# Performance work log

Hardware: AMD Instinct MI355X
Metric: run time of the kernel (lower is better)

## Reference

```python
import jax, jax.numpy as jnp
import numpy as np

B, T, H, C_CLS = 1024, 256, 256, 10
SIGMA = 1.0 / H


def setup_inputs() -> dict:
    key = jax.random.key(0)
    ks = jax.random.split(key, 10)
    n = lambda k, shp: SIGMA * jax.random.normal(k, shp, dtype=jnp.float32)
    return {
        "x": jax.random.normal(ks[0], (B, T), dtype=jnp.float32),
        "W_gx": n(ks[1], (1, H)), "W_gh": n(ks[2], (H, H)), "b_g": jnp.zeros(H, jnp.float32),
        "W_ix": n(ks[3], (1, H)), "W_ih": n(ks[4], (H, H)), "b_i": jnp.zeros(H, jnp.float32),
        "W_fx": n(ks[5], (1, H)), "W_fh": n(ks[6], (H, H)), "b_f": jnp.zeros(H, jnp.float32),
        "W_ox": n(ks[7], (1, H)), "W_oh": n(ks[8], (H, H)), "b_o": jnp.zeros(H, jnp.float32),
        "W_ph": n(ks[9], (H, C_CLS)), "b_p": jnp.zeros(C_CLS, jnp.float32),
    }


def reference(x, W_gx, W_gh, b_g, W_ix, W_ih, b_i, W_fx, W_fh, b_f, W_ox, W_oh, b_o, W_ph, b_p):
    batch = x.shape[0]
    hdim = W_gh.shape[0]

    def step(carry, x_t):
        h, c = carry
        xi = x_t[:, None]  # [B,1] scalar input per step
        g = jnp.tanh(xi @ W_gx + h @ W_gh + b_g)
        i = jax.nn.sigmoid(xi @ W_ix + h @ W_ih + b_i)
        # NOTE: original torch code swaps b_o/b_f in f_t/o_t; preserved faithfully.
        f = jax.nn.sigmoid(xi @ W_fx + h @ W_fh + b_o)
        o = jax.nn.sigmoid(xi @ W_ox + h @ W_oh + b_f)
        c = g * i + c * f
        h = jnp.tanh(c) * o
        return (h, c), None

    h0 = jnp.zeros((batch, hdim), x.dtype)
    c0 = jnp.zeros((batch, hdim), x.dtype)
    (h_T, _), _ = jax.lax.scan(step, (h0, c0), x.T)  # scan over time [T,B]
    # original computes p_t every step but only returns the last one
    return h_T @ W_ph + b_p
```

## Files before the change

kernel.cpp:

```cpp
#include <hip/hip_runtime.h>


#define Bsz   1024
#define Tt    256
#define Hh    256
#define NCLS  10
#define NTHR  512
#define WSPN  32768

typedef float f32x4 __attribute__((ext_vector_type(4)));
typedef short s16x8 __attribute__((ext_vector_type(8)));
typedef unsigned int u32;

__device__ __forceinline__ unsigned short f2bf(float f) {
    u32 u = __builtin_bit_cast(u32, f);
    return (unsigned short)((u + 0x7FFFu + ((u >> 16) & 1u)) >> 16);
}
__device__ __forceinline__ float bf2f(unsigned short b) {
    u32 u = ((u32)b) << 16;
    return __builtin_bit_cast(float, u);
}
template<int CTRL>
__device__ __forceinline__ float quadf(float v) {
    return __builtin_bit_cast(float,
        __builtin_amdgcn_update_dpp(0, __builtin_bit_cast(int, v),
                                    CTRL, 0xF, 0xF, true));
}
__device__ __forceinline__ float fast_tanh(float v) {
    const float e = __expf(-2.0f * fabsf(v));
    const float t = (1.0f - e) * __builtin_amdgcn_rcpf(1.0f + e);
    return copysignf(t, v);
}

extern "C" __global__ void __launch_bounds__(256)
lstm_prep(const float* __restrict__ W_gh, const float* __restrict__ W_ih,
          const float* __restrict__ W_fh, const float* __restrict__ W_oh,
          short* __restrict__ wsp)
{
    const int idx  = blockIdx.x * 256 + threadIdx.x;
    const int lane = idx & 63;
    const int ks   = (idx >> 6) & 7;
    const int wv   = (idx >> 9) & 7;
    const int cg   = idx >> 12;
    const int gate = lane & 3;
    const int hcol_g = cg * 32 + wv * 4 + ((lane & 15) >> 2);
    const int krow = lane >> 4;
    const float* __restrict__ Wg =
        (gate == 0) ? W_gh : (gate == 1) ? W_ih : (gate == 2) ? W_fh : W_oh;
    s16x8 v1, v2;
    #pragma unroll
    for (int e = 0; e < 8; ++e) {
        const float w = Wg[(size_t)(ks * 32 + krow * 8 + e) * Hh + hcol_g];
        const unsigned short c1 = f2bf(w);
        const unsigned short c2 = f2bf(w - bf2f(c1));
        v1[e] = (short)c1; v2[e] = (short)c2;
    }
    *(s16x8*)(wsp + (size_t)idx * 8)          = v1;
    *(s16x8*)(wsp + (size_t)(WSPN + idx) * 8) = v2;
}

extern "C" __global__ void __launch_bounds__(NTHR, 2)
lstm_step(const float* __restrict__ x,
          const float* __restrict__ W_gx, const float* __restrict__ b_g,
          const float* __restrict__ W_ix, const float* __restrict__ b_i,
          const float* __restrict__ W_fx, const float* __restrict__ b_f,
          const float* __restrict__ W_ox, const float* __restrict__ b_o,
          const short* __restrict__ wsp,
          const u32* __restrict__ hcur, u32* __restrict__ hnxt,
          float* __restrict__ cst, int t)
{
    __shared__ __align__(16) char smem[32768];

    const int tid  = threadIdx.x;
    const int lane = tid & 63;
    const int wv   = tid >> 6;
    const int cg   = blockIdx.x & 7;
    const int rg   = blockIdx.x >> 3;
    const int r0   = rg * 32;

    const int gate   = lane & 3;
    const int hcol_g = cg * 32 + wv * 4 + ((lane & 15) >> 2);
    const int krow   = lane >> 4;

    const s16x8* __restrict__ W1 =
        (const s16x8*)wsp + ((size_t)(cg * 8 + wv) * 8 * 64 + lane);
    s16x8 bw1[8], bw2[8];
    #pragma unroll
    for (int ks = 0; ks < 8; ++ks) {
        bw1[ks] = W1[ks * 64];
        bw2[ks] = W1[WSPN + ks * 64];
    }

    const float wx = ((gate == 0) ? W_gx : (gate == 1) ? W_ix : (gate == 2) ? W_fx : W_ox)[hcol_g];
    const float bb = ((gate == 0) ? b_g  : (gate == 1) ? b_i  : (gate == 2) ? b_o  : b_f )[hcol_g];

    float cold[2][4], xv[2][4];
    #pragma unroll
    for (int half = 0; half < 2; ++half)
        #pragma unroll
        for (int r = 0; r < 4; ++r) {
            const int row = r0 + half * 16 + krow * 4 + r;
            cold[half][r] = cst[(size_t)row * Hh + hcol_g];
            xv[half][r]   = x[(size_t)row * Tt + t];
        }

    const int sr = lane & 15;
    const int c8 = (lane >> 4) * 8;
    #pragma unroll
    for (int half = 0; half < 2; ++half) {
        const u32* src = hcur + (size_t)(r0 + half * 16 + sr) * Hh + wv * 32 + c8;
        const uint4 a = *(const uint4*)src;
        const uint4 b = *(const uint4*)(src + 4);
        u32 lo[4], hi[4];
        lo[0] = (a.x & 0xffffu) | (a.y << 16);  hi[0] = (a.x >> 16) | (a.y & 0xffff0000u);
        lo[1] = (a.z & 0xffffu) | (a.w << 16);  hi[1] = (a.z >> 16) | (a.w & 0xffff0000u);
        lo[2] = (b.x & 0xffffu) | (b.y << 16);  hi[2] = (b.x >> 16) | (b.y & 0xffff0000u);
        lo[3] = (b.z & 0xffffu) | (b.w << 16);  hi[3] = (b.z >> 16) | (b.w & 0xffff0000u);
        char* pb = smem + half * 16384 + wv * 1024 + lane * 16;
        *(uint4*)pb          = *(uint4*)lo;
        *(uint4*)(pb + 8192) = *(uint4*)hi;
    }
    __syncthreads();

    #pragma unroll
    for (int half = 0; half < 2; ++half) {
        f32x4 aA = {0.f,0.f,0.f,0.f}, aB = {0.f,0.f,0.f,0.f}, aC = {0.f,0.f,0.f,0.f};
        #pragma unroll
        for (int ks = 0; ks < 8; ++ks) {
            const char* ab = smem + half * 16384 + ks * 1024 + lane * 16;
            const s16x8 a1 = *(const s16x8*)ab;
            const s16x8 a2 = *(const s16x8*)(ab + 8192);
            aA = __builtin_amdgcn_mfma_f32_16x16x32_bf16(a1, bw1[ks], aA, 0, 0, 0);
            aB = __builtin_amdgcn_mfma_f32_16x16x32_bf16(a2, bw1[ks], aB, 0, 0, 0);
            aC = __builtin_amdgcn_mfma_f32_16x16x32_bf16(a1, bw2[ks], aC, 0, 0, 0);
        }
        const f32x4 acc = aA + aB + aC;

        #pragma unroll
        for (int r = 0; r < 4; ++r) {
            const int row = r0 + half * 16 + krow * 4 + r;
            const float pre = acc[r] + fmaf(xv[half][r], wx, bb);
            const float vin = (gate == 0) ? 2.0f * pre : pre;
            const float e   = __expf(-fabsf(vin));
            const float rc  = __builtin_amdgcn_rcpf(1.0f + e);
            const float sig = (vin >= 0.0f) ? rc : 1.0f - rc;
            const float th  = copysignf((1.0f - e) * rc, pre);
            const float act = (gate == 0) ? th : sig;
            const float gv = quadf<0x00>(act);
            const float iv = quadf<0x55>(act);
            const float fv = quadf<0xAA>(act);
            const float ov = quadf<0xFF>(act);
            const float cnew = fmaf(gv, iv, cold[half][r] * fv);
            const float hv   = fast_tanh(cnew) * ov;
            if (gate == 0) {
                cst[(size_t)row * Hh + hcol_g] = cnew;
                const unsigned short h1 = f2bf(hv);
                const unsigned short h2 = f2bf(hv - bf2f(h1));
                hnxt[(size_t)row * Hh + hcol_g] = (u32)h1 | ((u32)h2 << 16);
            }
        }
    }
}

extern "C" __global__ void __launch_bounds__(256)
lstm_head(const u32* __restrict__ hT, const float* __restrict__ W_ph,
          const float* __restrict__ b_p, float* __restrict__ out)
{
    __shared__ u32 tile[32 * Hh];
    const int tid = threadIdx.x;
    const int r0  = blockIdx.x * 32;
    for (int i = tid; i < 32 * Hh; i += 256)
        tile[i] = hT[(size_t)r0 * Hh + i];
    __syncthreads();
    for (int idx = tid; idx < 32 * NCLS; idx += 256) {
        const int row = idx / NCLS;
        const int cc  = idx - row * NCLS;
        float a = b_p[cc];
        for (int k = 0; k < Hh; ++k) {
            const u32 p = tile[row * Hh + k];
            a = fmaf(bf2f((unsigned short)p) + bf2f((unsigned short)(p >> 16)),
                     W_ph[k * NCLS + cc], a);
        }
        out[(size_t)(r0 + row) * NCLS + cc] = a;
    }
}

extern "C" void kernel_launch(void* const* d_in, const int* in_sizes, int n_in,
                              void* d_out, int out_size, void* d_ws, size_t ws_size,
                              hipStream_t stream) {
    const float* x    = (const float*)d_in[0];
    const float* W_gx = (const float*)d_in[1];
    const float* W_gh = (const float*)d_in[2];
    const float* b_g  = (const float*)d_in[3];
    const float* W_ix = (const float*)d_in[4];
    const float* W_ih = (const float*)d_in[5];
    const float* b_i  = (const float*)d_in[6];
    const float* W_fx = (const float*)d_in[7];
    const float* W_fh = (const float*)d_in[8];
    const float* b_f  = (const float*)d_in[9];
    const float* W_ox = (const float*)d_in[10];
    const float* W_oh = (const float*)d_in[11];
    const float* b_o  = (const float*)d_in[12];
    const float* W_ph = (const float*)d_in[13];
    const float* b_p  = (const float*)d_in[14];
    float* out = (float*)d_out;

    u32*   hbuf0 = (u32*)d_ws;
    u32*   hbuf1 = (u32*)((char*)d_ws + (1u << 20));
    float* cst   = (float*)((char*)d_ws + (2u << 20));
    short* wsp   = (short*)((char*)d_ws + (3u << 20));

    hipMemsetAsync(d_ws, 0, 3u << 20, stream);

    lstm_prep<<<dim3(128), dim3(256), 0, stream>>>(W_gh, W_ih, W_fh, W_oh, wsp);

    for (int t = 0; t < Tt; ++t) {
        const u32* hcur = (t & 1) ? hbuf1 : hbuf0;
        u32*       hnxt = (t & 1) ? hbuf0 : hbuf1;
        lstm_step<<<dim3(256), dim3(NTHR), 0, stream>>>(
            x, W_gx, b_g, W_ix, b_i, W_fx, b_f, W_ox, b_o,
            wsp, hcur, hnxt, cst, t);
    }

    lstm_head<<<dim3(32), dim3(256), 0, stream>>>(hbuf0, W_ph, b_p, out);
}
```

Baseline: 1.752 ms.

## Store hidden state in MFMA-ready split-bf16 layout and pre-transpose x

The step kernel now writes h in the exact shared-memory tile layout the next step's MFMA reads, staged through an LDS buffer. The next step can then load it with a plain contiguous copy instead of unpacking hi/lo planes from row-major data. x is transposed once in the prep kernel so each step reads 32 contiguous values instead of strided ones. The cost is an extra LDS staging pass and barrier per step, and a more complex indexing scheme in the head kernel.

```diff
diff --git a/kernel.cpp b/kernel.cpp
--- a/kernel.cpp
+++ b/kernel.cpp
@@ -35,41 +35,52 @@
 extern "C" __global__ void __launch_bounds__(256)
 lstm_prep(const float* __restrict__ W_gh, const float* __restrict__ W_ih,
           const float* __restrict__ W_fh, const float* __restrict__ W_oh,
-          short* __restrict__ wsp)
+          const float* __restrict__ x,
+          short* __restrict__ wsp, float* __restrict__ xT)
 {
-    const int idx  = blockIdx.x * 256 + threadIdx.x;
-    const int lane = idx & 63;
-    const int ks   = (idx >> 6) & 7;
-    const int wv   = (idx >> 9) & 7;
-    const int cg   = idx >> 12;
-    const int gate = lane & 3;
-    const int hcol_g = cg * 32 + wv * 4 + ((lane & 15) >> 2);
-    const int krow = lane >> 4;
-    const float* __restrict__ Wg =
-        (gate == 0) ? W_gh : (gate == 1) ? W_ih : (gate == 2) ? W_fh : W_oh;
-    s16x8 v1, v2;
-    #pragma unroll
-    for (int e = 0; e < 8; ++e) {
-        const float w = Wg[(size_t)(ks * 32 + krow * 8 + e) * Hh + hcol_g];
-        const unsigned short c1 = f2bf(w);
-        const unsigned short c2 = f2bf(w - bf2f(c1));
-        v1[e] = (short)c1; v2[e] = (short)c2;
-    }
-    *(s16x8*)(wsp + (size_t)idx * 8)          = v1;
-    *(s16x8*)(wsp + (size_t)(WSPN + idx) * 8) = v2;
+    const int bid = blockIdx.x;
+    if (bid < 128) {
+        const int idx  = bid * 256 + threadIdx.x;
+        const int lane = idx & 63;
+        const int ks   = (idx >> 6) & 7;
+        const int wv   = (idx >> 9) & 7;
+        const int cg   = idx >> 12;
+        const int gate = lane & 3;
+        const int hcol_g = cg * 32 + wv * 4 + ((lane & 15) >> 2);
+        const int krow = lane >> 4;
+        const float* __restrict__ Wg =
+            (gate == 0) ? W_gh : (gate == 1) ? W_ih : (gate == 2) ? W_fh : W_oh;
+        s16x8 v1, v2;
+        #pragma unroll
+        for (int e = 0; e < 8; ++e) {
+            const float w = Wg[(size_t)(ks * 32 + krow * 8 + e) * Hh + hcol_g];
+            const unsigned short c1 = f2bf(w);
+            const unsigned short c2 = f2bf(w - bf2f(c1));
+            v1[e] = (short)c1; v2[e] = (short)c2;
+        }
+        *(s16x8*)(wsp + (size_t)idx * 8)          = v1;
+        *(s16x8*)(wsp + (size_t)(WSPN + idx) * 8) = v2;
+    } else {
+        const int idx = (bid - 128) * 256 + threadIdx.x;
+        const int t   = idx >> 10;
+        const int row = idx & 1023;
+        xT[(size_t)t * Bsz + row] = x[(size_t)row * Tt + t];
+    }
 }
 
 extern "C" __global__ void __launch_bounds__(NTHR, 2)
-lstm_step(const float* __restrict__ x,
+lstm_step(const float* __restrict__ xT,
           const float* __restrict__ W_gx, const float* __restrict__ b_g,
           const float* __restrict__ W_ix, const float* __restrict__ b_i,
           const float* __restrict__ W_fx, const float* __restrict__ b_f,
           const float* __restrict__ W_ox, const float* __restrict__ b_o,
           const short* __restrict__ wsp,
-          const u32* __restrict__ hcur, u32* __restrict__ hnxt,
+          const char* __restrict__ hcur, char* __restrict__ hnxt,
           float* __restrict__ cst, int t)
 {
     __shared__ __align__(16) char smem[32768];
+    __shared__ u32   hown[32 * 33];
+    __shared__ float xsh[32];
 
     const int tid  = threadIdx.x;
     const int lane = tid & 63;
@@ -79,7 +90,8 @@
     const int r0   = rg * 32;
 
     const int gate   = lane & 3;
-    const int hcol_g = cg * 32 + wv * 4 + ((lane & 15) >> 2);
+    const int hcol_l = wv * 4 + ((lane & 15) >> 2);
+    const int hcol_g = cg * 32 + hcol_l;
     const int krow   = lane >> 4;
 
     const s16x8* __restrict__ W1 =
@@ -94,31 +106,22 @@
     const float wx = ((gate == 0) ? W_gx : (gate == 1) ? W_ix : (gate == 2) ? W_fx : W_ox)[hcol_g];
     const float bb = ((gate == 0) ? b_g  : (gate == 1) ? b_i  : (gate == 2) ? b_o  : b_f )[hcol_g];
 
-    float cold[2][4], xv[2][4];
+    float cold[2][4];
     #pragma unroll
     for (int half = 0; half < 2; ++half)
         #pragma unroll
-        for (int r = 0; r < 4; ++r) {
-            const int row = r0 + half * 16 + krow * 4 + r;
-            cold[half][r] = cst[(size_t)row * Hh + hcol_g];
-            xv[half][r]   = x[(size_t)row * Tt + t];
-        }
-
-    const int sr = lane & 15;
-    const int c8 = (lane >> 4) * 8;
-    #pragma unroll
-    for (int half = 0; half < 2; ++half) {
-        const u32* src = hcur + (size_t)(r0 + half * 16 + sr) * Hh + wv * 32 + c8;
-        const uint4 a = *(const uint4*)src;
-        const uint4 b = *(const uint4*)(src + 4);
-        u32 lo[4], hi[4];
-        lo[0] = (a.x & 0xffffu) | (a.y << 16);  hi[0] = (a.x >> 16) | (a.y & 0xffff0000u);
-        lo[1] = (a.z & 0xffffu) | (a.w << 16);  hi[1] = (a.z >> 16) | (a.w & 0xffff0000u);
-        lo[2] = (b.x & 0xffffu) | (b.y << 16);  hi[2] = (b.x >> 16) | (b.y & 0xffff0000u);
-        lo[3] = (b.z & 0xffffu) | (b.w << 16);  hi[3] = (b.z >> 16) | (b.w & 0xffff0000u);
-        char* pb = smem + half * 16384 + wv * 1024 + lane * 16;
-        *(uint4*)pb          = *(uint4*)lo;
-        *(uint4*)(pb + 8192) = *(uint4*)hi;
+        for (int r = 0; r < 4; ++r)
+            cold[half][r] = cst[(size_t)(r0 + half * 16 + krow * 4 + r) * Hh + hcol_g];
+
+    if (tid < 32) xsh[tid] = xT[(size_t)t * Bsz + r0 + tid];
+
+    {
+        const char* src = hcur + (size_t)rg * 32768;
+        #pragma unroll
+        for (int i = 0; i < 4; ++i) {
+            const int off = (tid + i * NTHR) * 16;
+            *(uint4*)(smem + off) = *(const uint4*)(src + off);
+        }
     }
     __syncthreads();
 
@@ -138,8 +141,8 @@
 
         #pragma unroll
         for (int r = 0; r < 4; ++r) {
-            const int row = r0 + half * 16 + krow * 4 + r;
-            const float pre = acc[r] + fmaf(xv[half][r], wx, bb);
+            const int rowl = half * 16 + krow * 4 + r;
+            const float pre = acc[r] + fmaf(xsh[rowl], wx, bb);
             const float vin = (gate == 0) ? 2.0f * pre : pre;
             const float e   = __expf(-fabsf(vin));
             const float rc  = __builtin_amdgcn_rcpf(1.0f + e);
@@ -153,35 +156,59 @@
             const float cnew = fmaf(gv, iv, cold[half][r] * fv);
             const float hv   = fast_tanh(cnew) * ov;
             if (gate == 0) {
-                cst[(size_t)row * Hh + hcol_g] = cnew;
+                cst[(size_t)(r0 + rowl) * Hh + hcol_g] = cnew;
                 const unsigned short h1 = f2bf(hv);
                 const unsigned short h2 = f2bf(hv - bf2f(h1));
-                hnxt[(size_t)row * Hh + hcol_g] = (u32)h1 | ((u32)h2 << 16);
+                hown[rowl * 33 + hcol_l] = (u32)h1 | ((u32)h2 << 16);
             }
         }
     }
+    __syncthreads();
+
+    if (tid < 256) {
+        const int half  = tid >> 7;
+        const int plane = (tid >> 6) & 1;
+        const int l     = tid & 63;
+        const int rowl  = half * 16 + (l & 15);
+        u32 w4[4];
+        #pragma unroll
+        for (int j = 0; j < 4; ++j) {
+            const u32 pa = hown[rowl * 33 + (l >> 4) * 8 + 2 * j];
+            const u32 pb = hown[rowl * 33 + (l >> 4) * 8 + 2 * j + 1];
+            const u32 va = plane ? (pa >> 16) : (pa & 0xffffu);
+            const u32 vb = plane ? (pb >> 16) : (pb & 0xffffu);
+            w4[j] = va | (vb << 16);
+        }
+        *(uint4*)(hnxt + (size_t)rg * 32768 + half * 16384 + plane * 8192
+                       + cg * 1024 + l * 16) = *(uint4*)w4;
+    }
 }
 
 extern "C" __global__ void __launch_bounds__(256)
-lstm_head(const u32* __restrict__ hT, const float* __restrict__ W_ph,
+lstm_head(const char* __restrict__ hT, const float* __restrict__ W_ph,
           const float* __restrict__ b_p, float* __restrict__ out)
 {
-    __shared__ u32 tile[32 * Hh];
+    __shared__ __align__(16) char tile[32768];
     const int tid = threadIdx.x;
-    const int r0  = blockIdx.x * 32;
-    for (int i = tid; i < 32 * Hh; i += 256)
-        tile[i] = hT[(size_t)r0 * Hh + i];
+    const int rg  = blockIdx.x;
+    const char* src = hT + (size_t)rg * 32768;
+    for (int i = tid; i < 2048; i += 256)
+        *(uint4*)(tile + i * 16) = *(const uint4*)(src + i * 16);
     __syncthreads();
     for (int idx = tid; idx < 32 * NCLS; idx += 256) {
-        const int row = idx / NCLS;
-        const int cc  = idx - row * NCLS;
+        const int rowl = idx / NCLS;
+        const int cc   = idx - rowl * NCLS;
+        const int half = rowl >> 4;
+        const int l4   = rowl & 15;
         float a = b_p[cc];
         for (int k = 0; k < Hh; ++k) {
-            const u32 p = tile[row * Hh + k];
-            a = fmaf(bf2f((unsigned short)p) + bf2f((unsigned short)(p >> 16)),
-                     W_ph[k * NCLS + cc], a);
-        }
-        out[(size_t)(r0 + row) * NCLS + cc] = a;
+            const int lane = ((k >> 3) & 3) * 16 + l4;
+            const int off  = half * 16384 + (k >> 5) * 1024 + lane * 16 + (k & 7) * 2;
+            const unsigned short lo = *(const unsigned short*)(tile + off);
+            const unsigned short hi = *(const unsigned short*)(tile + off + 8192);
+            a = fmaf(bf2f(lo) + bf2f(hi), W_ph[k * NCLS + cc], a);
+        }
+        out[(size_t)(rg * 32 + rowl) * NCLS + cc] = a;
     }
 }
 
@@ -205,22 +232,24 @@
     const float* b_p  = (const float*)d_in[14];
     float* out = (float*)d_out;
 
-    u32*   hbuf0 = (u32*)d_ws;
-    u32*   hbuf1 = (u32*)((char*)d_ws + (1u << 20));
-    float* cst   = (float*)((char*)d_ws + (2u << 20));
-    short* wsp   = (short*)((char*)d_ws + (3u << 20));
+    char*  hs0 = (char*)d_ws;
+    char*  hs1 = (char*)d_ws + (1u << 20);
+    float* cst = (float*)((char*)d_ws + (2u << 20));
+    short* wsp = (short*)((char*)d_ws + (3u << 20));
+    float* xT  = (float*)((char*)d_ws + (3u << 20) + (1u << 20));
 
     hipMemsetAsync(d_ws, 0, 3u << 20, stream);
 
-    lstm_prep<<<dim3(128), dim3(256), 0, stream>>>(W_gh, W_ih, W_fh, W_oh, wsp);
+    lstm_prep<<<dim3(128 + 1024), dim3(256), 0, stream>>>(
+        W_gh, W_ih, W_fh, W_oh, x, wsp, xT);
 
     for (int t = 0; t < Tt; ++t) {
-        const u32* hcur = (t & 1) ? hbuf1 : hbuf0;
-        u32*       hnxt = (t & 1) ? hbuf0 : hbuf1;
+        const char* hcur = (t & 1) ? hs1 : hs0;
+        char*       hnxt = (t & 1) ? hs0 : hs1;
         lstm_step<<<dim3(256), dim3(NTHR), 0, stream>>>(
-            x, W_gx, b_g, W_ix, b_i, W_fx, b_f, W_ox, b_o,
+            xT, W_gx, b_g, W_ix, b_i, W_fx, b_f, W_ox, b_o,
             wsp, hcur, hnxt, cst, t);
     }
 
-    lstm_head<<<dim3(32), dim3(256), 0, stream>>>(hbuf0, W_ph, b_p, out);
-}
+    lstm_head<<<dim3(32), dim3(256), 0, stream>>>(hs0, W_ph, b_p, out);
+}
```

Result: slower. 1.959 ms (+11.8%).
